# Kernel optimization log

Measured on AMD Instinct MI355X. Metric: run time of the kernel, lower is better.

## Reference

```python
import jax, jax.numpy as jnp
import numpy as np

N, E = 50000, 600000
D_IN, D_H, D_OUT = 512, 128, 1
BN_EPS = 1e-5


def setup_inputs() -> dict:
    key = jax.random.key(0)
    ks = jax.random.split(key, 16)
    s = 0.05
    inp = {
        "feature": jax.random.normal(ks[0], (N, D_IN), dtype=jnp.float32),
        "edge_index": jax.random.randint(ks[1], (2, E), 0, N, dtype=jnp.int32),
        "head_W": jax.random.normal(ks[2], (D_IN, D_H), dtype=jnp.float32) * s,
        "head_b": jnp.zeros((D_H,), dtype=jnp.float32),
        "gin_W1": jax.random.normal(ks[3], (D_H, D_H), dtype=jnp.float32) * s,
        "gin_b1": jnp.zeros((D_H,), dtype=jnp.float32),
        "lin_W1": jax.random.normal(ks[4], (D_H, D_H), dtype=jnp.float32) * s,
        "lin_b1": jnp.zeros((D_H,), dtype=jnp.float32),
        "gin_W2": jax.random.normal(ks[5], (D_H, D_H), dtype=jnp.float32) * s,
        "gin_b2": jnp.zeros((D_H,), dtype=jnp.float32),
        "lin_W2": jax.random.normal(ks[6], (D_H, D_H), dtype=jnp.float32) * s,
        "lin_b2": jnp.zeros((D_H,), dtype=jnp.float32),
        "tail_W": jax.random.normal(ks[7], (D_H, D_OUT), dtype=jnp.float32) * s,
        "tail_b": jnp.zeros((D_OUT,), dtype=jnp.float32),
        "bn_gamma": jnp.ones((D_OUT,), dtype=jnp.float32),
        "bn_beta": jnp.zeros((D_OUT,), dtype=jnp.float32),
    }
    return inp


def _gin_layer(x, src, dst, gin_W, gin_b, lin_W, lin_b):
    # PyG GINConv, eps=0: nn((1+eps)*x + sum_{j in N(i)} x_j)
    agg = jax.ops.segment_sum(x[src], dst, num_segments=N)  # [N, D_H]
    h = jax.nn.relu((x + agg) @ gin_W + gin_b)              # GIN MLP (dropout p=0)
    return h @ lin_W + lin_b                                # plain post-linear


def reference(feature, edge_index, head_W, head_b,
              gin_W1, gin_b1, lin_W1, lin_b1,
              gin_W2, gin_b2, lin_W2, lin_b2,
              tail_W, tail_b, bn_gamma, bn_beta):
    src, dst = edge_index[0], edge_index[1]
    x = jax.nn.relu(feature @ head_W + head_b)              # head block (dropout p=0)
    x = _gin_layer(x, src, dst, gin_W1, gin_b1, lin_W1, lin_b1)
    x = _gin_layer(x, src, dst, gin_W2, gin_b2, lin_W2, lin_b2)
    z = x @ tail_W + tail_b                                 # [N, 1]
    # BatchNorm1d in training mode: biased batch stats over the node dim
    mu = jnp.mean(z, axis=0, keepdims=True)
    var = jnp.mean((z - mu) ** 2, axis=0, keepdims=True)
    return (z - mu) * jax.lax.rsqrt(var + BN_EPS) * bn_gamma + bn_beta
```

## Files before the change

### kernel.cpp

```cpp
#include <hip/hip_runtime.h>

#define N_NODES 50000
#define N_EDGES 600000
#define DH 128
#define BN_EPS 1e-5f
#define SCAN_BLOCKS ((N_NODES + 255) / 256)

typedef __attribute__((ext_vector_type(8))) short bf16x8;
typedef __attribute__((ext_vector_type(4))) float f32x4;

__device__ inline unsigned short f2bf(float x) {
  unsigned u = __float_as_uint(x);
  return (unsigned short)((u + 0x7FFFu + ((u >> 16) & 1u)) >> 16);
}
__device__ inline float bf2f(unsigned short h) {
  return __uint_as_float(((unsigned)h) << 16);
}

__device__ inline void gl_lds16(const unsigned short* g, unsigned short* l) {
  __builtin_amdgcn_global_load_lds(
      (const __attribute__((address_space(1))) unsigned int*)g,
      (__attribute__((address_space(3))) unsigned int*)l, 16, 0, 0);
}

__global__ __launch_bounds__(256) void convert_W5(
    const float* __restrict__ hW, const float* __restrict__ g1,
    const float* __restrict__ l1, const float* __restrict__ g2,
    const float* __restrict__ l2,
    unsigned short* __restrict__ hH, unsigned short* __restrict__ hL,
    unsigned short* __restrict__ g1H, unsigned short* __restrict__ g1L,
    unsigned short* __restrict__ l1H, unsigned short* __restrict__ l1L,
    unsigned short* __restrict__ g2H, unsigned short* __restrict__ g2L,
    unsigned short* __restrict__ l2H, unsigned short* __restrict__ l2L) {
  int b = blockIdx.x;
  const float* W;
  unsigned short *hi, *lo;
  int idx;
  if (b < 256) {
    W = hW; hi = hH; lo = hL;
    idx = b * 256 + threadIdx.x;
  } else {
    int w = (b - 256) >> 6;
    idx = ((b - 256) & 63) * 256 + threadIdx.x;
    W = (w == 0) ? g1 : (w == 1) ? l1 : (w == 2) ? g2 : l2;
    hi = (w == 0) ? g1H : (w == 1) ? l1H : (w == 2) ? g2H : l2H;
    lo = (w == 0) ? g1L : (w == 1) ? l1L : (w == 2) ? g2L : l2L;
  }
  int k = idx >> 7;
  int n = idx & 127;
  float x = W[idx];
  unsigned short h = f2bf(x);
  unsigned short l = f2bf(x - bf2f(h));
  int kstep = k >> 5;
  int ctile = n >> 4;
  int lane = ((k >> 3) & 3) * 16 + (n & 15);
  int j = k & 7;
  size_t off = ((size_t)(kstep * 8 + ctile) * 64 + lane) * 8 + j;
  hi[off] = h;
  lo[off] = l;
}

__global__ __launch_bounds__(256) void to_bf16(const float* __restrict__ x,
                                               unsigned short* __restrict__ xb) {
  int i = blockIdx.x * 256 + threadIdx.x;
  if (i >= N_NODES * DH / 4) return;
  float4 v = ((const float4*)x)[i];
  ushort4 o;
  o.x = f2bf(v.x); o.y = f2bf(v.y); o.z = f2bf(v.z); o.w = f2bf(v.w);
  ((ushort4*)xb)[i] = o;
}

__global__ __launch_bounds__(256) void gemm_head(const float* __restrict__ A,
                                                 const unsigned short* __restrict__ Bh,
                                                 const unsigned short* __restrict__ Bl,
                                                 const float* __restrict__ bias,
                                                 float* __restrict__ C, int M) {
  constexpr int K = 512;
  constexpr int KSTEPS = K / 64;
  constexpr int ASTR = 72;
  __shared__ __align__(16) unsigned short Ah[64 * ASTR];
  __shared__ __align__(16) unsigned short Bhs[2][4096];
  __shared__ __align__(16) unsigned short Bls[2][4096];

  const int tid = threadIdx.x;
  const int wave = tid >> 6;
  const int lane = tid & 63;
  const int m0 = blockIdx.x * 64;

  const int s_row = tid >> 2;
  const int s_grp = tid & 3;
  const int g_row = m0 + s_row;
  const int g_rowc = (g_row < M) ? g_row : (M - 1);
  const float* af = A + (size_t)g_rowc * K + s_grp * 16;

  const int rgrp = wave & 1;
  const int ch = wave >> 1;

  f32x4 acc[2][4];
#pragma unroll
  for (int r = 0; r < 2; ++r)
#pragma unroll
    for (int c = 0; c < 4; ++c) acc[r][c] = (f32x4){0.f, 0.f, 0.f, 0.f};

  for (int ks = 0; ks < KSTEPS; ++ks) {
    {
      float4 f0 = *(const float4*)(af + ks * 64);
      float4 f1 = *(const float4*)(af + ks * 64 + 4);
      float4 f2 = *(const float4*)(af + ks * 64 + 8);
      float4 f3 = *(const float4*)(af + ks * 64 + 12);
      ushort4 h0, h1, h2, h3;
      h0.x = f2bf(f0.x); h0.y = f2bf(f0.y); h0.z = f2bf(f0.z); h0.w = f2bf(f0.w);
      h1.x = f2bf(f1.x); h1.y = f2bf(f1.y); h1.z = f2bf(f1.z); h1.w = f2bf(f1.w);
      h2.x = f2bf(f2.x); h2.y = f2bf(f2.y); h2.z = f2bf(f2.z); h2.w = f2bf(f2.w);
      h3.x = f2bf(f3.x); h3.y = f2bf(f3.y); h3.z = f2bf(f3.z); h3.w = f2bf(f3.w);
      int base = s_row * ASTR + s_grp * 16;
      *(ushort4*)&Ah[base + 0] = h0;
      *(ushort4*)&Ah[base + 4] = h1;
      *(ushort4*)&Ah[base + 8] = h2;
      *(ushort4*)&Ah[base + 12] = h3;
    }
#pragma unroll
    for (int s = 0; s < 2; ++s) {
      const unsigned short* sh = Bh + (size_t)(2 * ks + s) * 4096 + wave * 1024;
      const unsigned short* sl = Bl + (size_t)(2 * ks + s) * 4096 + wave * 1024;
      gl_lds16(sh + lane * 8, &Bhs[s][wave * 1024]);
      gl_lds16(sh + 512 + lane * 8, &Bhs[s][wave * 1024 + 512]);
      gl_lds16(sl + lane * 8, &Bls[s][wave * 1024]);
      gl_lds16(sl + 512 + lane * 8, &Bls[s][wave * 1024 + 512]);
    }
    __syncthreads();

#pragma unroll
    for (int s = 0; s < 2; ++s) {
      bf16x8 a0 = *(const bf16x8*)&Ah[(rgrp * 32 + (lane & 15)) * ASTR + s * 32 + (lane >> 4) * 8];
      bf16x8 a1 = *(const bf16x8*)&Ah[(rgrp * 32 + 16 + (lane & 15)) * ASTR + s * 32 + (lane >> 4) * 8];
#pragma unroll
      for (int c = 0; c < 4; ++c) {
        int ct = ch * 4 + c;
        bf16x8 bh = *(const bf16x8*)&Bhs[s][(ct * 64 + lane) * 8];
        bf16x8 bl = *(const bf16x8*)&Bls[s][(ct * 64 + lane) * 8];
        acc[0][c] = __builtin_amdgcn_mfma_f32_16x16x32_bf16(a0, bh, acc[0][c], 0, 0, 0);
        acc[0][c] = __builtin_amdgcn_mfma_f32_16x16x32_bf16(a0, bl, acc[0][c], 0, 0, 0);
        acc[1][c] = __builtin_amdgcn_mfma_f32_16x16x32_bf16(a1, bh, acc[1][c], 0, 0, 0);
        acc[1][c] = __builtin_amdgcn_mfma_f32_16x16x32_bf16(a1, bl, acc[1][c], 0, 0, 0);
      }
    }
    __syncthreads();
  }

  const int coln = lane & 15;
  const int rown = (lane >> 4) * 4;
#pragma unroll
  for (int c = 0; c < 4; ++c) {
    int colg = (ch * 4 + c) * 16 + coln;
    float bv = bias[colg];
#pragma unroll
    for (int r = 0; r < 2; ++r) {
#pragma unroll
      for (int reg = 0; reg < 4; ++reg) {
        int row = m0 + rgrp * 32 + r * 16 + rown + reg;
        if (row < M) {
          float v = fmaxf(acc[r][c][reg] + bv, 0.f);
          C[(size_t)row * DH + colg] = v;
        }
      }
    }
  }
}

__global__ __launch_bounds__(256) void gemm_gin(
    const unsigned short* __restrict__ yb,
    const unsigned short* __restrict__ B1h, const unsigned short* __restrict__ B1l,
    const float* __restrict__ b1,
    const unsigned short* __restrict__ B2h, const unsigned short* __restrict__ B2l,
    const float* __restrict__ b2, float* __restrict__ X, int M) {
  constexpr int K = 128;
  constexpr int KSTEPS = K / 32;
  constexpr int ASTR = 40;
  constexpr int HSTR = 136;
  __shared__ __align__(16) unsigned short Ah[64 * ASTR];
  __shared__ __align__(16) unsigned short Bhs[4096];
  __shared__ __align__(16) unsigned short Bls[4096];
  __shared__ __align__(16) unsigned short Hb[64 * HSTR];

  const int tid = threadIdx.x;
  const int wave = tid >> 6;
  const int lane = tid & 63;
  const int m0 = blockIdx.x * 64;

  const int s_row = tid >> 2;
  const int s_oct = tid & 3;
  const int g_row = m0 + s_row;
  const int g_rowc = (g_row < M) ? g_row : (M - 1);
  const unsigned short* ab = yb + (size_t)g_rowc * K + s_oct * 8;

  const int rgrp = wave & 1;
  const int ch = wave >> 1;
  const int coln = lane & 15;
  const int rown = (lane >> 4) * 4;

  auto issueB = [&](const unsigned short* Bh, const unsigned short* Bl, int ks) {
    const unsigned short* sh = Bh + (size_t)ks * 4096 + wave * 1024;
    const unsigned short* sl = Bl + (size_t)ks * 4096 + wave * 1024;
    gl_lds16(sh + lane * 8, &Bhs[wave * 1024]);
    gl_lds16(sh + 512 + lane * 8, &Bhs[wave * 1024 + 512]);
    gl_lds16(sl + lane * 8, &Bls[wave * 1024]);
    gl_lds16(sl + 512 + lane * 8, &Bls[wave * 1024 + 512]);
  };

  f32x4 acc[2][4];
#pragma unroll
  for (int r = 0; r < 2; ++r)
#pragma unroll
    for (int c = 0; c < 4; ++c) acc[r][c] = (f32x4){0.f, 0.f, 0.f, 0.f};

  for (int ks = 0; ks < KSTEPS; ++ks) {
    *(uint4*)&Ah[s_row * ASTR + s_oct * 8] = *(const uint4*)(ab + ks * 32);
    issueB(B1h, B1l, ks);
    __syncthreads();
    bf16x8 a0 = *(const bf16x8*)&Ah[(rgrp * 32 + (lane & 15)) * ASTR + (lane >> 4) * 8];
    bf16x8 a1 = *(const bf16x8*)&Ah[(rgrp * 32 + 16 + (lane & 15)) * ASTR + (lane >> 4) * 8];
#pragma unroll
    for (int c = 0; c < 4; ++c) {
      int ct = ch * 4 + c;
      bf16x8 bh = *(const bf16x8*)&Bhs[(ct * 64 + lane) * 8];
      bf16x8 bl = *(const bf16x8*)&Bls[(ct * 64 + lane) * 8];
      acc[0][c] = __builtin_amdgcn_mfma_f32_16x16x32_bf16(a0, bh, acc[0][c], 0, 0, 0);
      acc[0][c] = __builtin_amdgcn_mfma_f32_16x16x32_bf16(a0, bl, acc[0][c], 0, 0, 0);
      acc[1][c] = __builtin_amdgcn_mfma_f32_16x16x32_bf16(a1, bh, acc[1][c], 0, 0, 0);
      acc[1][c] = __builtin_amdgcn_mfma_f32_16x16x32_bf16(a1, bl, acc[1][c], 0, 0, 0);
    }
    __syncthreads();
  }

#pragma unroll
  for (int c = 0; c < 4; ++c) {
    int colg = (ch * 4 + c) * 16 + coln;
    float bv = b1[colg];
#pragma unroll
    for (int r = 0; r < 2; ++r) {
#pragma unroll
      for (int reg = 0; reg < 4; ++reg) {
        int lrow = rgrp * 32 + r * 16 + rown + reg;
        float v = fmaxf(acc[r][c][reg] + bv, 0.f);
        Hb[lrow * HSTR + colg] = f2bf(v);
      }
      acc[r][c] = (f32x4){0.f, 0.f, 0.f, 0.f};
    }
  }

  for (int ks = 0; ks < KSTEPS; ++ks) {
    issueB(B2h, B2l, ks);
    __syncthreads();
    bf16x8 a0 = *(const bf16x8*)&Hb[(rgrp * 32 + (lane & 15)) * HSTR + ks * 32 + (lane >> 4) * 8];
    bf16x8 a1 = *(const bf16x8*)&Hb[(rgrp * 32 + 16 + (lane & 15)) * HSTR + ks * 32 + (lane >> 4) * 8];
#pragma unroll
    for (int c = 0; c < 4; ++c) {
      int ct = ch * 4 + c;
      bf16x8 bh = *(const bf16x8*)&Bhs[(ct * 64 + lane) * 8];
      bf16x8 bl = *(const bf16x8*)&Bls[(ct * 64 + lane) * 8];
      acc[0][c] = __builtin_amdgcn_mfma_f32_16x16x32_bf16(a0, bh, acc[0][c], 0, 0, 0);
      acc[0][c] = __builtin_amdgcn_mfma_f32_16x16x32_bf16(a0, bl, acc[0][c], 0, 0, 0);
      acc[1][c] = __builtin_amdgcn_mfma_f32_16x16x32_bf16(a1, bh, acc[1][c], 0, 0, 0);
      acc[1][c] = __builtin_amdgcn_mfma_f32_16x16x32_bf16(a1, bl, acc[1][c], 0, 0, 0);
    }
    __syncthreads();
  }

#pragma unroll
  for (int c = 0; c < 4; ++c) {
    int colg = (ch * 4 + c) * 16 + coln;
    float bv = b2[colg];
#pragma unroll
    for (int r = 0; r < 2; ++r) {
#pragma unroll
      for (int reg = 0; reg < 4; ++reg) {
        int row = m0 + rgrp * 32 + r * 16 + rown + reg;
        if (row < M) X[(size_t)row * DH + colg] = acc[r][c][reg] + bv;
      }
    }
  }
}

__global__ __launch_bounds__(256) void count_deg(const int* __restrict__ eidx,
                                                 int* __restrict__ cnt) {
  int e = blockIdx.x * 256 + threadIdx.x;
  if (e < N_EDGES) atomicAdd(&cnt[eidx[N_EDGES + e]], 1);
}

__global__ __launch_bounds__(256) void scan_block(const int* __restrict__ cnt,
                                                  int* __restrict__ rs,
                                                  int* __restrict__ partials) {
  int t = threadIdx.x;
  int i = blockIdx.x * 256 + t;
  int v = (i < N_NODES) ? cnt[i] : 0;
  __shared__ int s[256];
  s[t] = v;
  __syncthreads();
#pragma unroll
  for (int off = 1; off < 256; off <<= 1) {
    int add = (t >= off) ? s[t - off] : 0;
    __syncthreads();
    s[t] += add;
    __syncthreads();
  }
  if (i < N_NODES) rs[i] = s[t] - v;
  if (t == 255) partials[blockIdx.x] = s[255];
}

__global__ __launch_bounds__(256) void scan_partials(int* __restrict__ partials) {
  int t = threadIdx.x;
  int v = (t < SCAN_BLOCKS) ? partials[t] : 0;
  __shared__ int s[256];
  s[t] = v;
  __syncthreads();
#pragma unroll
  for (int off = 1; off < 256; off <<= 1) {
    int add = (t >= off) ? s[t - off] : 0;
    __syncthreads();
    s[t] += add;
    __syncthreads();
  }
  if (t < SCAN_BLOCKS) partials[t] = s[t] - v;
}

__global__ __launch_bounds__(256) void add_offsets(int* __restrict__ rs,
                                                   const int* __restrict__ partials) {
  int i = blockIdx.x * 256 + threadIdx.x;
  if (i < N_NODES) rs[i] += partials[blockIdx.x];
  if (i == 0) rs[N_NODES] = N_EDGES;
}

__global__ __launch_bounds__(256) void fill_csr(const int* __restrict__ eidx,
                                                const int* __restrict__ rs,
                                                int* __restrict__ cursor,
                                                int* __restrict__ esrc) {
  int e = blockIdx.x * 256 + threadIdx.x;
  if (e >= N_EDGES) return;
  int d = eidx[N_EDGES + e];
  int p = atomicAdd(&cursor[d], 1);
  esrc[rs[d] + p] = eidx[e];
}

__global__ __launch_bounds__(256) void gin_aggregate_bf16(
    const unsigned short* __restrict__ xb, const float* __restrict__ x,
    const int* __restrict__ rs, const int* __restrict__ esrc,
    unsigned* __restrict__ yb) {
  int node = blockIdx.x * 4 + (threadIdx.x >> 6);
  int lane = threadIdx.x & 63;
  if (node >= N_NODES) return;
  float2 acc = ((const float2*)x)[(size_t)node * 64 + lane];
  const unsigned* xb2 = (const unsigned*)xb;
  int beg = rs[node];
  int end = rs[node + 1];
  int j = beg;
  for (; j + 4 <= end; j += 4) {
    int s0 = esrc[j + 0];
    int s1 = esrc[j + 1];
    int s2 = esrc[j + 2];
    int s3 = esrc[j + 3];
    unsigned v0 = xb2[(size_t)s0 * 64 + lane];
    unsigned v1 = xb2[(size_t)s1 * 64 + lane];
    unsigned v2 = xb2[(size_t)s2 * 64 + lane];
    unsigned v3 = xb2[(size_t)s3 * 64 + lane];
    acc.x += (__uint_as_float(v0 << 16) + __uint_as_float(v1 << 16)) +
             (__uint_as_float(v2 << 16) + __uint_as_float(v3 << 16));
    acc.y += (__uint_as_float(v0 & 0xFFFF0000u) + __uint_as_float(v1 & 0xFFFF0000u)) +
             (__uint_as_float(v2 & 0xFFFF0000u) + __uint_as_float(v3 & 0xFFFF0000u));
  }
  for (; j < end; ++j) {
    unsigned v = xb2[(size_t)esrc[j] * 64 + lane];
    acc.x += __uint_as_float(v << 16);
    acc.y += __uint_as_float(v & 0xFFFF0000u);
  }
  yb[(size_t)node * 64 + lane] =
      (unsigned)f2bf(acc.x) | ((unsigned)f2bf(acc.y) << 16);
}

__global__ __launch_bounds__(256) void tail_bn1(const float* __restrict__ x,
                                                const float* __restrict__ tw,
                                                const float* __restrict__ tb,
                                                float* __restrict__ z,
                                                float* __restrict__ red) {
  const int lane = threadIdx.x & 31;
  const int grp = threadIdx.x >> 5;
  float4 w = *(const float4*)(tw + lane * 4);
  float accS = 0.f, accQ = 0.f;
  for (int node = blockIdx.x * 8 + grp; node < N_NODES; node += gridDim.x * 8) {
    float4 v = *(const float4*)(x + (size_t)node * DH + lane * 4);
    float p = v.x * w.x + v.y * w.y + v.z * w.z + v.w * w.w;
#pragma unroll
    for (int m = 16; m; m >>= 1) p += __shfl_xor(p, m, 32);
    if (lane == 0) {
      float zv = p + tb[0];
      z[node] = zv;
      accS += zv;
      accQ += zv * zv;
    }
  }
  __shared__ float sS[256];
  __shared__ float sQ[256];
  sS[threadIdx.x] = accS;
  sQ[threadIdx.x] = accQ;
  __syncthreads();
  for (int s = 128; s; s >>= 1) {
    if (threadIdx.x < s) {
      sS[threadIdx.x] += sS[threadIdx.x + s];
      sQ[threadIdx.x] += sQ[threadIdx.x + s];
    }
    __syncthreads();
  }
  if (threadIdx.x == 0) {
    atomicAdd(&red[0], sS[0]);
    atomicAdd(&red[1], sQ[0]);
  }
}

__global__ __launch_bounds__(256) void bn2(const float* __restrict__ z,
                                           const float* __restrict__ red,
                                           const float* __restrict__ gamma,
                                           const float* __restrict__ beta,
                                           float* __restrict__ out) {
  int i = blockIdx.x * 256 + threadIdx.x;
  if (i >= N_NODES) return;
  float mu = red[0] * (1.0f / N_NODES);
  float var = red[1] * (1.0f / N_NODES) - mu * mu;
  out[i] = (z[i] - mu) * rsqrtf(var + BN_EPS) * gamma[0] + beta[0];
}

extern "C" void kernel_launch(void* const* d_in, const int* in_sizes, int n_in,
                              void* d_out, int out_size, void* d_ws, size_t ws_size,
                              hipStream_t stream) {
  const float* feature = (const float*)d_in[0];
  const int* eidx = (const int*)d_in[1];
  const float* head_W = (const float*)d_in[2];
  const float* head_b = (const float*)d_in[3];
  const float* gin_W1 = (const float*)d_in[4];
  const float* gin_b1 = (const float*)d_in[5];
  const float* lin_W1 = (const float*)d_in[6];
  const float* lin_b1 = (const float*)d_in[7];
  const float* gin_W2 = (const float*)d_in[8];
  const float* gin_b2 = (const float*)d_in[9];
  const float* lin_W2 = (const float*)d_in[10];
  const float* lin_b2 = (const float*)d_in[11];
  const float* tail_W = (const float*)d_in[12];
  const float* tail_b = (const float*)d_in[13];
  const float* bn_gamma = (const float*)d_in[14];
  const float* bn_beta = (const float*)d_in[15];

  float* X = (float*)d_ws;
  float* z = X + (size_t)N_NODES * DH;
  float* red = z + N_NODES;
  int* row_start = (int*)(red + 2);
  int* cnt = row_start + (N_NODES + 1);
  int* partials = cnt + N_NODES;
  int* esrc = partials + 256;
  unsigned short* wp =
      (unsigned short*)(((uintptr_t)(esrc + N_EDGES) + 15) & ~(uintptr_t)15);
  unsigned short* hH = wp;
  unsigned short* hL = hH + 65536;
  unsigned short* g1H = hL + 65536;
  unsigned short* g1L = g1H + 16384;
  unsigned short* l1H = g1L + 16384;
  unsigned short* l1L = l1H + 16384;
  unsigned short* g2H = l1L + 16384;
  unsigned short* g2L = g2H + 16384;
  unsigned short* l2H = g2L + 16384;
  unsigned short* l2L = l2H + 16384;
  unsigned short* xb = l2L + 16384;
  unsigned short* yb = xb + (size_t)N_NODES * DH;

  const int gemm_grid = (N_NODES + 63) / 64;
  const int edge_grid = (N_EDGES + 255) / 256;
  const int agg_grid = (N_NODES + 3) / 4;
  const int cvt_grid = (N_NODES * DH / 4 + 255) / 256;

  convert_W5<<<512, 256, 0, stream>>>(head_W, gin_W1, lin_W1, gin_W2, lin_W2,
                                      hH, hL, g1H, g1L, l1H, l1L, g2H, g2L,
                                      l2H, l2L);

  hipMemsetAsync(cnt, 0, N_NODES * sizeof(int), stream);
  hipMemsetAsync(red, 0, 2 * sizeof(float), stream);
  count_deg<<<edge_grid, 256, 0, stream>>>(eidx, cnt);
  scan_block<<<SCAN_BLOCKS, 256, 0, stream>>>(cnt, row_start, partials);
  scan_partials<<<1, 256, 0, stream>>>(partials);
  add_offsets<<<SCAN_BLOCKS, 256, 0, stream>>>(row_start, partials);
  hipMemsetAsync(cnt, 0, N_NODES * sizeof(int), stream);
  fill_csr<<<edge_grid, 256, 0, stream>>>(eidx, row_start, cnt, esrc);

  gemm_head<<<gemm_grid, 256, 0, stream>>>(feature, hH, hL, head_b, X, N_NODES);

  to_bf16<<<cvt_grid, 256, 0, stream>>>(X, xb);
  gin_aggregate_bf16<<<agg_grid, 256, 0, stream>>>(xb, X, row_start, esrc,
                                                   (unsigned*)yb);
  gemm_gin<<<gemm_grid, 256, 0, stream>>>(yb, g1H, g1L, gin_b1, l1H, l1L,
                                          lin_b1, X, N_NODES);

  to_bf16<<<cvt_grid, 256, 0, stream>>>(X, xb);
  gin_aggregate_bf16<<<agg_grid, 256, 0, stream>>>(xb, X, row_start, esrc,
                                                   (unsigned*)yb);
  gemm_gin<<<gemm_grid, 256, 0, stream>>>(yb, g2H, g2L, gin_b2, l2H, l2L,
                                          lin_b2, X, N_NODES);

  tail_bn1<<<256, 256, 0, stream>>>(X, tail_W, tail_b, z, red);
  bn2<<<(N_NODES + 255) / 256, 256, 0, stream>>>(z, red, bn_gamma, bn_beta, (float*)d_out);
}
```

Measured before the change: 424.4 us.

## Software-pipeline head and GIN GEMMs with double-buffered LDS and register prefetch

The head GEMM now runs in 32-wide K steps with double-buffered A and B tiles in LDS. The fp32 A rows for step ks+2 are prefetched into registers while step ks computes, and the B loads for the next step are issued asynchronously. The GIN GEMM loads its whole 64x128 A tile up front, double-buffers the B tiles, and prefetches the first B2 tile during the last B1 step. The aim is to hide global-load latency behind MFMA work and replace most __syncthreads with one barrier per step plus manual waitcnts. That manual vmcnt/lgkmcnt ordering is fragile and could introduce races if the compiler reorders memory operations.

Result: slower. 439.0 us (+3.4%).

```diff
diff --git a/kernel.cpp b/kernel.cpp
--- a/kernel.cpp
+++ b/kernel.cpp
@@ -76,9 +76,9 @@
                                                  const float* __restrict__ bias,
                                                  float* __restrict__ C, int M) {
   constexpr int K = 512;
-  constexpr int KSTEPS = K / 64;
-  constexpr int ASTR = 72;
-  __shared__ __align__(16) unsigned short Ah[64 * ASTR];
+  constexpr int KSTEPS = K / 32;
+  constexpr int ASTR = 40;
+  __shared__ __align__(16) unsigned short Ah[2][64 * ASTR];
   __shared__ __align__(16) unsigned short Bhs[2][4096];
   __shared__ __align__(16) unsigned short Bls[2][4096];
 
@@ -91,61 +91,74 @@
   const int s_grp = tid & 3;
   const int g_row = m0 + s_row;
   const int g_rowc = (g_row < M) ? g_row : (M - 1);
-  const float* af = A + (size_t)g_rowc * K + s_grp * 16;
+  const float* af = A + (size_t)g_rowc * K + s_grp * 8;
 
   const int rgrp = wave & 1;
   const int ch = wave >> 1;
 
+  auto issueB = [&](int ks, int buf) {
+    const unsigned short* sh = Bh + (size_t)ks * 4096 + wave * 1024;
+    const unsigned short* sl = Bl + (size_t)ks * 4096 + wave * 1024;
+    gl_lds16(sh + lane * 8, &Bhs[buf][wave * 1024]);
+    gl_lds16(sh + 512 + lane * 8, &Bhs[buf][wave * 1024 + 512]);
+    gl_lds16(sl + lane * 8, &Bls[buf][wave * 1024]);
+    gl_lds16(sl + 512 + lane * 8, &Bls[buf][wave * 1024 + 512]);
+  };
+
   f32x4 acc[2][4];
 #pragma unroll
   for (int r = 0; r < 2; ++r)
 #pragma unroll
     for (int c = 0; c < 4; ++c) acc[r][c] = (f32x4){0.f, 0.f, 0.f, 0.f};
 
+  float4 ar[2][2];
+  ar[0][0] = *(const float4*)(af + 0);
+  ar[0][1] = *(const float4*)(af + 4);
+  issueB(0, 0);
+  asm volatile("" ::: "memory");
+  ar[1][0] = *(const float4*)(af + 32);
+  ar[1][1] = *(const float4*)(af + 36);
+
+#pragma unroll
   for (int ks = 0; ks < KSTEPS; ++ks) {
+    const int cur = ks & 1;
+    if (ks < KSTEPS - 1)
+      asm volatile("s_waitcnt vmcnt(2)" ::: "memory");
+    else
+      asm volatile("s_waitcnt vmcnt(0)" ::: "memory");
+
     {
-      float4 f0 = *(const float4*)(af + ks * 64);
-      float4 f1 = *(const float4*)(af + ks * 64 + 4);
-      float4 f2 = *(const float4*)(af + ks * 64 + 8);
-      float4 f3 = *(const float4*)(af + ks * 64 + 12);
-      ushort4 h0, h1, h2, h3;
+      float4 f0 = ar[cur][0];
+      float4 f1 = ar[cur][1];
+      ushort4 h0, h1;
       h0.x = f2bf(f0.x); h0.y = f2bf(f0.y); h0.z = f2bf(f0.z); h0.w = f2bf(f0.w);
       h1.x = f2bf(f1.x); h1.y = f2bf(f1.y); h1.z = f2bf(f1.z); h1.w = f2bf(f1.w);
-      h2.x = f2bf(f2.x); h2.y = f2bf(f2.y); h2.z = f2bf(f2.z); h2.w = f2bf(f2.w);
-      h3.x = f2bf(f3.x); h3.y = f2bf(f3.y); h3.z = f2bf(f3.z); h3.w = f2bf(f3.w);
-      int base = s_row * ASTR + s_grp * 16;
-      *(ushort4*)&Ah[base + 0] = h0;
-      *(ushort4*)&Ah[base + 4] = h1;
-      *(ushort4*)&Ah[base + 8] = h2;
-      *(ushort4*)&Ah[base + 12] = h3;
-    }
-#pragma unroll
-    for (int s = 0; s < 2; ++s) {
-      const unsigned short* sh = Bh + (size_t)(2 * ks + s) * 4096 + wave * 1024;
-      const unsigned short* sl = Bl + (size_t)(2 * ks + s) * 4096 + wave * 1024;
-      gl_lds16(sh + lane * 8, &Bhs[s][wave * 1024]);
-      gl_lds16(sh + 512 + lane * 8, &Bhs[s][wave * 1024 + 512]);
-      gl_lds16(sl + lane * 8, &Bls[s][wave * 1024]);
-      gl_lds16(sl + 512 + lane * 8, &Bls[s][wave * 1024 + 512]);
-    }
-    __syncthreads();
-
-#pragma unroll
-    for (int s = 0; s < 2; ++s) {
-      bf16x8 a0 = *(const bf16x8*)&Ah[(rgrp * 32 + (lane & 15)) * ASTR + s * 32 + (lane >> 4) * 8];
-      bf16x8 a1 = *(const bf16x8*)&Ah[(rgrp * 32 + 16 + (lane & 15)) * ASTR + s * 32 + (lane >> 4) * 8];
-#pragma unroll
-      for (int c = 0; c < 4; ++c) {
-        int ct = ch * 4 + c;
-        bf16x8 bh = *(const bf16x8*)&Bhs[s][(ct * 64 + lane) * 8];
-        bf16x8 bl = *(const bf16x8*)&Bls[s][(ct * 64 + lane) * 8];
-        acc[0][c] = __builtin_amdgcn_mfma_f32_16x16x32_bf16(a0, bh, acc[0][c], 0, 0, 0);
-        acc[0][c] = __builtin_amdgcn_mfma_f32_16x16x32_bf16(a0, bl, acc[0][c], 0, 0, 0);
-        acc[1][c] = __builtin_amdgcn_mfma_f32_16x16x32_bf16(a1, bh, acc[1][c], 0, 0, 0);
-        acc[1][c] = __builtin_amdgcn_mfma_f32_16x16x32_bf16(a1, bl, acc[1][c], 0, 0, 0);
-      }
-    }
-    __syncthreads();
+      int base = s_row * ASTR + s_grp * 8;
+      *(ushort4*)&Ah[cur][base + 0] = h0;
+      *(ushort4*)&Ah[cur][base + 4] = h1;
+    }
+    asm volatile("s_waitcnt lgkmcnt(0)" ::: "memory");
+    __builtin_amdgcn_s_barrier();
+
+    if (ks + 1 < KSTEPS) issueB(ks + 1, cur ^ 1);
+    asm volatile("" ::: "memory");
+    if (ks + 2 < KSTEPS) {
+      ar[cur][0] = *(const float4*)(af + (ks + 2) * 32);
+      ar[cur][1] = *(const float4*)(af + (ks + 2) * 32 + 4);
+    }
+
+    bf16x8 a0 = *(const bf16x8*)&Ah[cur][(rgrp * 32 + (lane & 15)) * ASTR + (lane >> 4) * 8];
+    bf16x8 a1 = *(const bf16x8*)&Ah[cur][(rgrp * 32 + 16 + (lane & 15)) * ASTR + (lane >> 4) * 8];
+#pragma unroll
+    for (int c = 0; c < 4; ++c) {
+      int ct = ch * 4 + c;
+      bf16x8 bh = *(const bf16x8*)&Bhs[cur][(ct * 64 + lane) * 8];
+      bf16x8 bl = *(const bf16x8*)&Bls[cur][(ct * 64 + lane) * 8];
+      acc[0][c] = __builtin_amdgcn_mfma_f32_16x16x32_bf16(a0, bh, acc[0][c], 0, 0, 0);
+      acc[0][c] = __builtin_amdgcn_mfma_f32_16x16x32_bf16(a0, bl, acc[0][c], 0, 0, 0);
+      acc[1][c] = __builtin_amdgcn_mfma_f32_16x16x32_bf16(a1, bh, acc[1][c], 0, 0, 0);
+      acc[1][c] = __builtin_amdgcn_mfma_f32_16x16x32_bf16(a1, bl, acc[1][c], 0, 0, 0);
+    }
   }
 
   const int coln = lane & 15;
@@ -174,14 +187,11 @@
     const float* __restrict__ b1,
     const unsigned short* __restrict__ B2h, const unsigned short* __restrict__ B2l,
     const float* __restrict__ b2, float* __restrict__ X, int M) {
-  constexpr int K = 128;
-  constexpr int KSTEPS = K / 32;
-  constexpr int ASTR = 40;
+  constexpr int KSTEPS = 4;
   constexpr int HSTR = 136;
-  __shared__ __align__(16) unsigned short Ah[64 * ASTR];
-  __shared__ __align__(16) unsigned short Bhs[4096];
-  __shared__ __align__(16) unsigned short Bls[4096];
-  __shared__ __align__(16) unsigned short Hb[64 * HSTR];
+  __shared__ __align__(16) unsigned short AH[64 * HSTR];
+  __shared__ __align__(16) unsigned short Bhs[2][4096];
+  __shared__ __align__(16) unsigned short Bls[2][4096];
 
   const int tid = threadIdx.x;
   const int wave = tid >> 6;
@@ -189,23 +199,24 @@
   const int m0 = blockIdx.x * 64;
 
   const int s_row = tid >> 2;
-  const int s_oct = tid & 3;
+  const int s_grp = tid & 3;
   const int g_row = m0 + s_row;
   const int g_rowc = (g_row < M) ? g_row : (M - 1);
-  const unsigned short* ab = yb + (size_t)g_rowc * K + s_oct * 8;
+  const unsigned short* ab = yb + (size_t)g_rowc * DH + s_grp * 32;
 
   const int rgrp = wave & 1;
   const int ch = wave >> 1;
   const int coln = lane & 15;
   const int rown = (lane >> 4) * 4;
 
-  auto issueB = [&](const unsigned short* Bh, const unsigned short* Bl, int ks) {
+  auto issueB = [&](const unsigned short* Bh, const unsigned short* Bl, int ks,
+                    int buf) {
     const unsigned short* sh = Bh + (size_t)ks * 4096 + wave * 1024;
     const unsigned short* sl = Bl + (size_t)ks * 4096 + wave * 1024;
-    gl_lds16(sh + lane * 8, &Bhs[wave * 1024]);
-    gl_lds16(sh + 512 + lane * 8, &Bhs[wave * 1024 + 512]);
-    gl_lds16(sl + lane * 8, &Bls[wave * 1024]);
-    gl_lds16(sl + 512 + lane * 8, &Bls[wave * 1024 + 512]);
+    gl_lds16(sh + lane * 8, &Bhs[buf][wave * 1024]);
+    gl_lds16(sh + 512 + lane * 8, &Bhs[buf][wave * 1024 + 512]);
+    gl_lds16(sl + lane * 8, &Bls[buf][wave * 1024]);
+    gl_lds16(sl + 512 + lane * 8, &Bls[buf][wave * 1024 + 512]);
   };
 
   f32x4 acc[2][4];
@@ -214,25 +225,45 @@
 #pragma unroll
     for (int c = 0; c < 4; ++c) acc[r][c] = (f32x4){0.f, 0.f, 0.f, 0.f};
 
+  uint4 a0v = *(const uint4*)(ab + 0);
+  uint4 a1v = *(const uint4*)(ab + 8);
+  uint4 a2v = *(const uint4*)(ab + 16);
+  uint4 a3v = *(const uint4*)(ab + 24);
+  issueB(B1h, B1l, 0, 0);
+  {
+    int base = s_row * HSTR + s_grp * 32;
+    *(uint4*)&AH[base + 0] = a0v;
+    *(uint4*)&AH[base + 8] = a1v;
+    *(uint4*)&AH[base + 16] = a2v;
+    *(uint4*)&AH[base + 24] = a3v;
+  }
+  asm volatile("s_waitcnt lgkmcnt(0)" ::: "memory");
+
+#pragma unroll
   for (int ks = 0; ks < KSTEPS; ++ks) {
-    *(uint4*)&Ah[s_row * ASTR + s_oct * 8] = *(const uint4*)(ab + ks * 32);
-    issueB(B1h, B1l, ks);
-    __syncthreads();
-    bf16x8 a0 = *(const bf16x8*)&Ah[(rgrp * 32 + (lane & 15)) * ASTR + (lane >> 4) * 8];
-    bf16x8 a1 = *(const bf16x8*)&Ah[(rgrp * 32 + 16 + (lane & 15)) * ASTR + (lane >> 4) * 8];
+    const int cur = ks & 1;
+    asm volatile("s_waitcnt vmcnt(0)" ::: "memory");
+    __builtin_amdgcn_s_barrier();
+    if (ks + 1 < KSTEPS)
+      issueB(B1h, B1l, ks + 1, cur ^ 1);
+    else
+      issueB(B2h, B2l, 0, cur ^ 1);
+
+    bf16x8 a0 = *(const bf16x8*)&AH[(rgrp * 32 + (lane & 15)) * HSTR + ks * 32 + (lane >> 4) * 8];
+    bf16x8 a1 = *(const bf16x8*)&AH[(rgrp * 32 + 16 + (lane & 15)) * HSTR + ks * 32 + (lane >> 4) * 8];
 #pragma unroll
     for (int c = 0; c < 4; ++c) {
       int ct = ch * 4 + c;
-      bf16x8 bh = *(const bf16x8*)&Bhs[(ct * 64 + lane) * 8];
-      bf16x8 bl = *(const bf16x8*)&Bls[(ct * 64 + lane) * 8];
+      bf16x8 bh = *(const bf16x8*)&Bhs[cur][(ct * 64 + lane) * 8];
+      bf16x8 bl = *(const bf16x8*)&Bls[cur][(ct * 64 + lane) * 8];
       acc[0][c] = __builtin_amdgcn_mfma_f32_16x16x32_bf16(a0, bh, acc[0][c], 0, 0, 0);
       acc[0][c] = __builtin_amdgcn_mfma_f32_16x16x32_bf16(a0, bl, acc[0][c], 0, 0, 0);
       acc[1][c] = __builtin_amdgcn_mfma_f32_16x16x32_bf16(a1, bh, acc[1][c], 0, 0, 0);
       acc[1][c] = __builtin_amdgcn_mfma_f32_16x16x32_bf16(a1, bl, acc[1][c], 0, 0, 0);
     }
-    __syncthreads();
-  }
-
+  }
+
+  __builtin_amdgcn_s_barrier();
 #pragma unroll
   for (int c = 0; c < 4; ++c) {
     int colg = (ch * 4 + c) * 16 + coln;
@@ -243,28 +274,32 @@
       for (int reg = 0; reg < 4; ++reg) {
         int lrow = rgrp * 32 + r * 16 + rown + reg;
         float v = fmaxf(acc[r][c][reg] + bv, 0.f);
-        Hb[lrow * HSTR + colg] = f2bf(v);
+        AH[lrow * HSTR + colg] = f2bf(v);
       }
       acc[r][c] = (f32x4){0.f, 0.f, 0.f, 0.f};
     }
   }
-
+  asm volatile("s_waitcnt lgkmcnt(0)" ::: "memory");
+
+#pragma unroll
   for (int ks = 0; ks < KSTEPS; ++ks) {
-    issueB(B2h, B2l, ks);
-    __syncthreads();
-    bf16x8 a0 = *(const bf16x8*)&Hb[(rgrp * 32 + (lane & 15)) * HSTR + ks * 32 + (lane >> 4) * 8];
-    bf16x8 a1 = *(const bf16x8*)&Hb[(rgrp * 32 + 16 + (lane & 15)) * HSTR + ks * 32 + (lane >> 4) * 8];
+    const int cur = ks & 1;
+    asm volatile("s_waitcnt vmcnt(0)" ::: "memory");
+    __builtin_amdgcn_s_barrier();
+    if (ks + 1 < KSTEPS) issueB(B2h, B2l, ks + 1, cur ^ 1);
+
+    bf16x8 a0 = *(const bf16x8*)&AH[(rgrp * 32 + (lane & 15)) * HSTR + ks * 32 + (lane >> 4) * 8];
+    bf16x8 a1 = *(const bf16x8*)&AH[(rgrp * 32 + 16 + (lane & 15)) * HSTR + ks * 32 + (lane >> 4) * 8];
 #pragma unroll
     for (int c = 0; c < 4; ++c) {
       int ct = ch * 4 + c;
-      bf16x8 bh = *(const bf16x8*)&Bhs[(ct * 64 + lane) * 8];
-      bf16x8 bl = *(const bf16x8*)&Bls[(ct * 64 + lane) * 8];
+      bf16x8 bh = *(const bf16x8*)&Bhs[cur][(ct * 64 + lane) * 8];
+      bf16x8 bl = *(const bf16x8*)&Bls[cur][(ct * 64 + lane) * 8];
       acc[0][c] = __builtin_amdgcn_mfma_f32_16x16x32_bf16(a0, bh, acc[0][c], 0, 0, 0);
       acc[0][c] = __builtin_amdgcn_mfma_f32_16x16x32_bf16(a0, bl, acc[0][c], 0, 0, 0);
       acc[1][c] = __builtin_amdgcn_mfma_f32_16x16x32_bf16(a1, bh, acc[1][c], 0, 0, 0);
       acc[1][c] = __builtin_amdgcn_mfma_f32_16x16x32_bf16(a1, bl, acc[1][c], 0, 0, 0);
     }
-    __syncthreads();
   }
 
 #pragma unroll
```

## Fuse bf16 conversion into GEMM epilogues and vectorize output stores via column permutation

Applied to the files above, without the earlier changes.

The to_bf16 kernels are removed. The head and first GIN GEMMs now write the bf16 copy of their output directly in the epilogue. The weight packing permutes output columns so that each lane owns 4 contiguous columns, which allows float4/ushort4 stores instead of scalar strided stores. The aggregation loop also gains an 8-way unrolled gather to keep more loads in flight. This saves two full passes over the 50000x128 activation and cuts store instruction count, at the cost of a more intricate layout coupling between weight packing and the epilogue.

Result: faster. 399.0 us (-6.0%).

```diff
diff --git a/kernel.cpp b/kernel.cpp
--- a/kernel.cpp
+++ b/kernel.cpp
@@ -52,29 +52,22 @@
   unsigned short h = f2bf(x);
   unsigned short l = f2bf(x - bf2f(h));
   int kstep = k >> 5;
-  int ctile = n >> 4;
-  int lane = ((k >> 3) & 3) * 16 + (n & 15);
+  int ctile = ((n >> 6) << 2) | (n & 3);
+  int cs = (n >> 2) & 15;
+  int lane = ((k >> 3) & 3) * 16 + cs;
   int j = k & 7;
   size_t off = ((size_t)(kstep * 8 + ctile) * 64 + lane) * 8 + j;
   hi[off] = h;
   lo[off] = l;
 }
 
-__global__ __launch_bounds__(256) void to_bf16(const float* __restrict__ x,
-                                               unsigned short* __restrict__ xb) {
-  int i = blockIdx.x * 256 + threadIdx.x;
-  if (i >= N_NODES * DH / 4) return;
-  float4 v = ((const float4*)x)[i];
-  ushort4 o;
-  o.x = f2bf(v.x); o.y = f2bf(v.y); o.z = f2bf(v.z); o.w = f2bf(v.w);
-  ((ushort4*)xb)[i] = o;
-}
-
 __global__ __launch_bounds__(256) void gemm_head(const float* __restrict__ A,
                                                  const unsigned short* __restrict__ Bh,
                                                  const unsigned short* __restrict__ Bl,
                                                  const float* __restrict__ bias,
-                                                 float* __restrict__ C, int M) {
+                                                 float* __restrict__ C,
+                                                 unsigned short* __restrict__ xb_out,
+                                                 int M) {
   constexpr int K = 512;
   constexpr int KSTEPS = K / 64;
   constexpr int ASTR = 72;
@@ -150,19 +143,23 @@
 
   const int coln = lane & 15;
   const int rown = (lane >> 4) * 4;
-#pragma unroll
-  for (int c = 0; c < 4; ++c) {
-    int colg = (ch * 4 + c) * 16 + coln;
-    float bv = bias[colg];
-#pragma unroll
-    for (int r = 0; r < 2; ++r) {
-#pragma unroll
-      for (int reg = 0; reg < 4; ++reg) {
-        int row = m0 + rgrp * 32 + r * 16 + rown + reg;
-        if (row < M) {
-          float v = fmaxf(acc[r][c][reg] + bv, 0.f);
-          C[(size_t)row * DH + colg] = v;
-        }
+  const int colbase = ch * 64 + coln * 4;
+  const float4 bv = *(const float4*)(bias + colbase);
+#pragma unroll
+  for (int r = 0; r < 2; ++r) {
+#pragma unroll
+    for (int reg = 0; reg < 4; ++reg) {
+      int row = m0 + rgrp * 32 + r * 16 + rown + reg;
+      if (row < M) {
+        float4 v;
+        v.x = fmaxf(acc[r][0][reg] + bv.x, 0.f);
+        v.y = fmaxf(acc[r][1][reg] + bv.y, 0.f);
+        v.z = fmaxf(acc[r][2][reg] + bv.z, 0.f);
+        v.w = fmaxf(acc[r][3][reg] + bv.w, 0.f);
+        *(float4*)&C[(size_t)row * DH + colbase] = v;
+        ushort4 hb;
+        hb.x = f2bf(v.x); hb.y = f2bf(v.y); hb.z = f2bf(v.z); hb.w = f2bf(v.w);
+        *(ushort4*)&xb_out[(size_t)row * DH + colbase] = hb;
       }
     }
   }
@@ -173,7 +170,8 @@
     const unsigned short* __restrict__ B1h, const unsigned short* __restrict__ B1l,
     const float* __restrict__ b1,
     const unsigned short* __restrict__ B2h, const unsigned short* __restrict__ B2l,
-    const float* __restrict__ b2, float* __restrict__ X, int M) {
+    const float* __restrict__ b2, float* __restrict__ X,
+    unsigned short* __restrict__ xb_out, int M) {
   constexpr int K = 128;
   constexpr int KSTEPS = K / 32;
   constexpr int ASTR = 40;
@@ -198,6 +196,7 @@
   const int ch = wave >> 1;
   const int coln = lane & 15;
   const int rown = (lane >> 4) * 4;
+  const int colbase = ch * 64 + coln * 4;
 
   auto issueB = [&](const unsigned short* Bh, const unsigned short* Bl, int ks) {
     const unsigned short* sh = Bh + (size_t)ks * 4096 + wave * 1024;
@@ -233,20 +232,25 @@
     __syncthreads();
   }
 
-#pragma unroll
-  for (int c = 0; c < 4; ++c) {
-    int colg = (ch * 4 + c) * 16 + coln;
-    float bv = b1[colg];
+  {
+    const float4 bv = *(const float4*)(b1 + colbase);
 #pragma unroll
     for (int r = 0; r < 2; ++r) {
 #pragma unroll
       for (int reg = 0; reg < 4; ++reg) {
         int lrow = rgrp * 32 + r * 16 + rown + reg;
-        float v = fmaxf(acc[r][c][reg] + bv, 0.f);
-        Hb[lrow * HSTR + colg] = f2bf(v);
+        ushort4 hb;
+        hb.x = f2bf(fmaxf(acc[r][0][reg] + bv.x, 0.f));
+        hb.y = f2bf(fmaxf(acc[r][1][reg] + bv.y, 0.f));
+        hb.z = f2bf(fmaxf(acc[r][2][reg] + bv.z, 0.f));
+        hb.w = f2bf(fmaxf(acc[r][3][reg] + bv.w, 0.f));
+        *(ushort4*)&Hb[lrow * HSTR + colbase] = hb;
       }
-      acc[r][c] = (f32x4){0.f, 0.f, 0.f, 0.f};
-    }
+    }
+#pragma unroll
+    for (int r = 0; r < 2; ++r)
+#pragma unroll
+      for (int c = 0; c < 4; ++c) acc[r][c] = (f32x4){0.f, 0.f, 0.f, 0.f};
   }
 
   for (int ks = 0; ks < KSTEPS; ++ks) {
@@ -267,16 +271,26 @@
     __syncthreads();
   }
 
-#pragma unroll
-  for (int c = 0; c < 4; ++c) {
-    int colg = (ch * 4 + c) * 16 + coln;
-    float bv = b2[colg];
+  {
+    const float4 bv = *(const float4*)(b2 + colbase);
 #pragma unroll
     for (int r = 0; r < 2; ++r) {
 #pragma unroll
       for (int reg = 0; reg < 4; ++reg) {
         int row = m0 + rgrp * 32 + r * 16 + rown + reg;
-        if (row < M) X[(size_t)row * DH + colg] = acc[r][c][reg] + bv;
+        if (row < M) {
+          float4 v;
+          v.x = acc[r][0][reg] + bv.x;
+          v.y = acc[r][1][reg] + bv.y;
+          v.z = acc[r][2][reg] + bv.z;
+          v.w = acc[r][3][reg] + bv.w;
+          *(float4*)&X[(size_t)row * DH + colbase] = v;
+          if (xb_out) {
+            ushort4 hb;
+            hb.x = f2bf(v.x); hb.y = f2bf(v.y); hb.z = f2bf(v.z); hb.w = f2bf(v.w);
+            *(ushort4*)&xb_out[(size_t)row * DH + colbase] = hb;
+          }
+        }
       }
     }
   }
@@ -354,6 +368,32 @@
   int beg = rs[node];
   int end = rs[node + 1];
   int j = beg;
+  for (; j + 8 <= end; j += 8) {
+    int s0 = esrc[j + 0];
+    int s1 = esrc[j + 1];
+    int s2 = esrc[j + 2];
+    int s3 = esrc[j + 3];
+    int s4 = esrc[j + 4];
+    int s5 = esrc[j + 5];
+    int s6 = esrc[j + 6];
+    int s7 = esrc[j + 7];
+    unsigned v0 = xb2[(size_t)s0 * 64 + lane];
+    unsigned v1 = xb2[(size_t)s1 * 64 + lane];
+    unsigned v2 = xb2[(size_t)s2 * 64 + lane];
+    unsigned v3 = xb2[(size_t)s3 * 64 + lane];
+    unsigned v4 = xb2[(size_t)s4 * 64 + lane];
+    unsigned v5 = xb2[(size_t)s5 * 64 + lane];
+    unsigned v6 = xb2[(size_t)s6 * 64 + lane];
+    unsigned v7 = xb2[(size_t)s7 * 64 + lane];
+    acc.x += ((__uint_as_float(v0 << 16) + __uint_as_float(v1 << 16)) +
+              (__uint_as_float(v2 << 16) + __uint_as_float(v3 << 16))) +
+             ((__uint_as_float(v4 << 16) + __uint_as_float(v5 << 16)) +
+              (__uint_as_float(v6 << 16) + __uint_as_float(v7 << 16)));
+    acc.y += ((__uint_as_float(v0 & 0xFFFF0000u) + __uint_as_float(v1 & 0xFFFF0000u)) +
+              (__uint_as_float(v2 & 0xFFFF0000u) + __uint_as_float(v3 & 0xFFFF0000u))) +
+             ((__uint_as_float(v4 & 0xFFFF0000u) + __uint_as_float(v5 & 0xFFFF0000u)) +
+              (__uint_as_float(v6 & 0xFFFF0000u) + __uint_as_float(v7 & 0xFFFF0000u)));
+  }
   for (; j + 4 <= end; j += 4) {
     int s0 = esrc[j + 0];
     int s1 = esrc[j + 1];
@@ -473,7 +513,6 @@
   const int gemm_grid = (N_NODES + 63) / 64;
   const int edge_grid = (N_EDGES + 255) / 256;
   const int agg_grid = (N_NODES + 3) / 4;
-  const int cvt_grid = (N_NODES * DH / 4 + 255) / 256;
 
   convert_W5<<<512, 256, 0, stream>>>(head_W, gin_W1, lin_W1, gin_W2, lin_W2,
                                       hH, hL, g1H, g1L, l1H, l1L, g2H, g2L,
@@ -488,19 +527,18 @@
   hipMemsetAsync(cnt, 0, N_NODES * sizeof(int), stream);
   fill_csr<<<edge_grid, 256, 0, stream>>>(eidx, row_start, cnt, esrc);
 
-  gemm_head<<<gemm_grid, 256, 0, stream>>>(feature, hH, hL, head_b, X, N_NODES);
-
-  to_bf16<<<cvt_grid, 256, 0, stream>>>(X, xb);
+  gemm_head<<<gemm_grid, 256, 0, stream>>>(feature, hH, hL, head_b, X, xb,
+                                           N_NODES);
+
   gin_aggregate_bf16<<<agg_grid, 256, 0, stream>>>(xb, X, row_start, esrc,
                                                    (unsigned*)yb);
   gemm_gin<<<gemm_grid, 256, 0, stream>>>(yb, g1H, g1L, gin_b1, l1H, l1L,
-                                          lin_b1, X, N_NODES);
-
-  to_bf16<<<cvt_grid, 256, 0, stream>>>(X, xb);
+                                          lin_b1, X, xb, N_NODES);
+
   gin_aggregate_bf16<<<agg_grid, 256, 0, stream>>>(xb, X, row_start, esrc,
                                                    (unsigned*)yb);
   gemm_gin<<<gemm_grid, 256, 0, stream>>>(yb, g2H, g2L, gin_b2, l2H, l2L,
-                                          lin_b2, X, N_NODES);
+                                          lin_b2, X, nullptr, N_NODES);
 
   tail_bn1<<<256, 256, 0, stream>>>(X, tail_W, tail_b, z, red);
   bn2<<<(N_NODES + 255) / 256, 256, 0, stream>>>(z, red, bn_gamma, bn_beta, (float*)d_out);
```
